# Performance work log

Hardware: AMD Instinct MI355X
Metric: run time of the kernel (lower is better)

## Reference

```python
import jax, jax.numpy as jnp
import numpy as np

EPS = 1e-4  # ridge term added to W W^T before inversion


def setup_inputs() -> dict:
    key = jax.random.key(0)
    k1, k2 = jax.random.split(key)
    B, F, C, D = 4096, 2048, 100, 16
    x = jax.random.normal(k1, (B, F), dtype=jnp.float32)
    # match torch reset_parameters: uniform(-stdv, stdv), stdv = 1/sqrt(F)
    stdv = 1.0 / np.sqrt(F)
    weight = jax.random.uniform(k2, (C, D, F), dtype=jnp.float32, minval=-stdv, maxval=stdv)
    return {"x": x, "weight": weight}


def reference(x, weight):
    # weight: [C, D, F], x: [B, F]
    C, D, F = weight.shape
    # per-capsule Gram matrix W W^T : [C, D, D]
    weight_caps = jnp.einsum('cdf,cef->cde', weight, weight)
    sigma = jnp.linalg.inv(weight_caps + EPS * jnp.eye(D, dtype=weight.dtype))
    # u[b,c,d] = <x_b, W_{c,d}>  (the x @ W^T projection of the original)
    u = jnp.einsum('bf,cdf->bcd', x, weight)
    # original chain: (u @ sigma @ W) @ x == u^T sigma u  (same math, no [B,C,F] temp)
    out = jnp.einsum('bcd,cde,bce->bc', u, sigma, u)
    return jnp.sqrt(out)
```

## Files before the change

### kernel.cpp

```cpp
#include <hip/hip_runtime.h>
#include <hip/hip_bf16.h>
#include <math.h>

#define F_DIM 2048
#define B_DIM 4096
#define C_DIM 100
#define D_DIM 16
#define N_DIM (C_DIM*D_DIM)
#define N_PAD 1664
#define RIDGE_EPS 1e-4f

typedef __attribute__((ext_vector_type(8))) short bf16x8;
typedef __attribute__((ext_vector_type(4))) float f32x4;

__device__ __forceinline__ void gload16(const void* g, void* l) {
  __builtin_amdgcn_global_load_lds(
      (const __attribute__((address_space(1))) void*)g,
      (__attribute__((address_space(3))) void*)l,
      16, 0, 0);
}

#define VM_BAR(N) asm volatile("s_waitcnt vmcnt(" #N ")\n\ts_barrier" ::: "memory")
#define LGKM_BAR() asm volatile("s_waitcnt lgkmcnt(0)\n\ts_barrier" ::: "memory")

__device__ __forceinline__ unsigned short f2bf(float f) {
  unsigned u = __float_as_uint(f);
  u += 0x7FFFu + ((u >> 16) & 1u);
  return (unsigned short)(u >> 16);
}

__global__ __launch_bounds__(256) void cvt_gram_kernel(
    const float* __restrict__ x, const float* __restrict__ w,
    unsigned short* __restrict__ xb, unsigned short* __restrict__ wb,
    float* __restrict__ sigma, int nx8, int nw8, int npad8) {
  __shared__ float part[4][64][4];
  __shared__ float G[16][17];
  __shared__ float IV[16][17];
  int t = threadIdx.x;
  if (blockIdx.x < C_DIM) {
    int c = blockIdx.x;
    int lane = t & 63, wid = t >> 6;
    const float* src = w + (size_t)c * (D_DIM * F_DIM)
                         + (size_t)(lane & 15) * F_DIM + ((lane >> 4) * 8) + wid * 512;
    f32x4 g = {0.f, 0.f, 0.f, 0.f};
#pragma unroll
    for (int kt = 0; kt < 16; ++kt) {
      float4 v0 = *(const float4*)(src + kt * 32);
      float4 v1 = *(const float4*)(src + kt * 32 + 4);
      bf16x8 f;
      f[0] = (short)f2bf(v0.x); f[1] = (short)f2bf(v0.y);
      f[2] = (short)f2bf(v0.z); f[3] = (short)f2bf(v0.w);
      f[4] = (short)f2bf(v1.x); f[5] = (short)f2bf(v1.y);
      f[6] = (short)f2bf(v1.z); f[7] = (short)f2bf(v1.w);
      g = __builtin_amdgcn_mfma_f32_16x16x32_bf16(f, f, g, 0, 0, 0);
    }
#pragma unroll
    for (int j = 0; j < 4; j++) part[wid][lane][j] = g[j];
    int d = t >> 4, e = t & 15;
    IV[d][e] = (d == e) ? 1.f : 0.f;
    __syncthreads();
    if (t < 64) {
      int col = t & 15;
#pragma unroll
      for (int j = 0; j < 4; j++) {
        int row = (t >> 4) * 4 + j;
        float s4 = part[0][t][j] + part[1][t][j] + part[2][t][j] + part[3][t][j];
        G[row][col] = s4 + (row == col ? RIDGE_EPS : 0.f);
      }
    }
    __syncthreads();
    for (int k = 0; k < 16; k++) {
      float piv = G[k][k];
      float gke = G[k][e];
      float ike = IV[k][e];
      float f   = G[d][k];
      float gde = G[d][e];
      float ide = IV[d][e];
      __syncthreads();
      if (d == k) {
        G[k][e]  = gke / piv;
        IV[k][e] = ike / piv;
      } else {
        G[d][e]  = gde - f * gke / piv;
        IV[d][e] = ide - f * ike / piv;
      }
      __syncthreads();
    }
    sigma[(size_t)c * 256 + t] = IV[d][e];
    return;
  }
  int i = (blockIdx.x - C_DIM) * 256 + t;
  const float* in; unsigned short* outp; int idx;
  if (i < nx8) { in = x; outp = xb; idx = i; }
  else {
    idx = i - nx8;
    if (idx >= nw8) {
      int idx3 = idx - nw8;
      if (idx3 < npad8) {
        uint4 z = {0, 0, 0, 0};
        *((uint4*)(wb + (size_t)N_DIM * F_DIM) + idx3) = z;
      }
      return;
    }
    in = w; outp = wb;
  }
  const float4* p = (const float4*)in + (size_t)idx * 2;
  float4 a = p[0], b = p[1];
  float v[8] = {a.x, a.y, a.z, a.w, b.x, b.y, b.z, b.w};
  union { unsigned short u16[8]; uint4 u4; } r;
#pragma unroll
  for (int j = 0; j < 8; j++) r.u16[j] = f2bf(v[j]);
  *((uint4*)outp + idx) = r.u4;
}

__global__ __launch_bounds__(512) void gemm_caps_kernel(
    const unsigned short* __restrict__ xb,
    const unsigned short* __restrict__ wb,
    const float* __restrict__ sigma,
    float* __restrict__ out)
{
  __shared__ __align__(16) unsigned char smem[67584];
  const int t = threadIdx.x;
  const int lane = t & 63;
  const int wid = t >> 6;
  const int wr = wid >> 2, wc = wid & 3;
  const int bid = blockIdx.x;
  const int swz = (bid & 7) * 52 + (bid >> 3);
  const int bn = swz % 13;
  const int bm = swz / 13;
  const int rowBase = bm * 128;
  const int colBase = bn * 128;

  unsigned char* buf0 = smem;
  unsigned char* buf1 = smem + 32768;

  const unsigned short* srcA[2]; unsigned qA[2];
  const unsigned short* srcB[2]; unsigned qB[2];
#pragma unroll
  for (int i = 0; i < 2; i++) {
    unsigned q = (unsigned)wid * 1024u + (unsigned)i * 8192u + (unsigned)lane * 16u;
    unsigned r = q >> 7, b = q & 127u;
    unsigned cb = b ^ ((r & 7u) << 4);
    qA[i] = q;
    srcA[i] = xb + (size_t)(rowBase + (int)r) * F_DIM + (cb >> 1);
    qB[i] = 16384u + q;
    srcB[i] = wb + (size_t)(colBase + (int)r) * F_DIM + (cb >> 1);
  }

  int aOff[4][2], bOff[2][2];
#pragma unroll
  for (int m = 0; m < 4; m++) {
    int r = wr * 64 + m * 16 + (lane & 15);
    int sw = (r & 7) << 4;
#pragma unroll
    for (int ks = 0; ks < 2; ks++) {
      int kb = ks * 64 + ((lane >> 4) << 4);
      aOff[m][ks] = r * 128 + (kb ^ sw);
    }
  }
#pragma unroll
  for (int n = 0; n < 2; n++) {
    int r = wc * 32 + n * 16 + (lane & 15);
    int sw = (r & 7) << 4;
#pragma unroll
    for (int ks = 0; ks < 2; ks++) {
      int kb = ks * 64 + ((lane >> 4) << 4);
      bOff[n][ks] = 16384 + r * 128 + (kb ^ sw);
    }
  }

  f32x4 acc[4][2];
#pragma unroll
  for (int m = 0; m < 4; m++)
#pragma unroll
    for (int n = 0; n < 2; n++)
      acc[m][n] = (f32x4){0.f, 0.f, 0.f, 0.f};

  auto stage = [&](unsigned char* buf, int kt) {
    const size_t koff = (size_t)kt * 64;
#pragma unroll
    for (int i = 0; i < 2; i++) gload16(srcA[i] + koff, buf + qA[i]);
#pragma unroll
    for (int i = 0; i < 2; i++) gload16(srcB[i] + koff, buf + qB[i]);
  };
  auto compute = [&](const unsigned char* buf) {
#pragma unroll
    for (int ks = 0; ks < 2; ks++) {
      bf16x8 a0 = *(const bf16x8*)(buf + aOff[0][ks]);
      bf16x8 a1 = *(const bf16x8*)(buf + aOff[1][ks]);
      bf16x8 a2 = *(const bf16x8*)(buf + aOff[2][ks]);
      bf16x8 a3 = *(const bf16x8*)(buf + aOff[3][ks]);
      bf16x8 b0 = *(const bf16x8*)(buf + bOff[0][ks]);
      bf16x8 b1 = *(const bf16x8*)(buf + bOff[1][ks]);
      acc[0][0] = __builtin_amdgcn_mfma_f32_16x16x32_bf16(a0, b0, acc[0][0], 0, 0, 0);
      acc[0][1] = __builtin_amdgcn_mfma_f32_16x16x32_bf16(a0, b1, acc[0][1], 0, 0, 0);
      acc[1][0] = __builtin_amdgcn_mfma_f32_16x16x32_bf16(a1, b0, acc[1][0], 0, 0, 0);
      acc[1][1] = __builtin_amdgcn_mfma_f32_16x16x32_bf16(a1, b1, acc[1][1], 0, 0, 0);
      acc[2][0] = __builtin_amdgcn_mfma_f32_16x16x32_bf16(a2, b0, acc[2][0], 0, 0, 0);
      acc[2][1] = __builtin_amdgcn_mfma_f32_16x16x32_bf16(a2, b1, acc[2][1], 0, 0, 0);
      acc[3][0] = __builtin_amdgcn_mfma_f32_16x16x32_bf16(a3, b0, acc[3][0], 0, 0, 0);
      acc[3][1] = __builtin_amdgcn_mfma_f32_16x16x32_bf16(a3, b1, acc[3][1], 0, 0, 0);
    }
  };

  stage(buf0, 0);
  for (int kt = 0; kt < 30; kt += 2) {
    stage(buf1, kt + 1);
    VM_BAR(4);
    compute(buf0);
    LGKM_BAR();
    stage(buf0, kt + 2);
    VM_BAR(4);
    compute(buf1);
    LGKM_BAR();
  }
  stage(buf1, 31);
  VM_BAR(4);
  compute(buf0);
  LGKM_BAR();
  VM_BAR(0);
  compute(buf1);
  LGKM_BAR();

  float* uT = (float*)smem;
#pragma unroll
  for (int m = 0; m < 4; m++)
#pragma unroll
    for (int n = 0; n < 2; n++)
#pragma unroll
      for (int j = 0; j < 4; j++) {
        int row = wr * 64 + m * 16 + ((lane >> 4) << 2) + j;
        int col = wc * 32 + n * 16 + (lane & 15);
        uT[row * 132 + col] = acc[m][n][j];
      }
  __syncthreads();
  const int capBase = bn * 8;
#pragma unroll
  for (int pp = 0; pp < 2; ++pp) {
    int pi = t + pp * 512;
    int row = pi & 127;
    int cl = __builtin_amdgcn_readfirstlane(pi >> 7);
    const float* uu = uT + row * 132 + cl * 16;
    f32x4 u0 = *(const f32x4*)(uu + 0);
    f32x4 u1 = *(const f32x4*)(uu + 4);
    f32x4 u2 = *(const f32x4*)(uu + 8);
    f32x4 u3 = *(const f32x4*)(uu + 12);
    float ur[16];
#pragma unroll
    for (int j = 0; j < 4; j++) { ur[j] = u0[j]; ur[4+j] = u1[j]; ur[8+j] = u2[j]; ur[12+j] = u3[j]; }
    int cap = capBase + cl;
    const float* s = sigma + (size_t)cap * 256;
    float qf = 0.f;
#pragma unroll
    for (int dd = 0; dd < 16; ++dd) {
      float td = 0.5f * s[dd * 16 + dd] * ur[dd];
#pragma unroll
      for (int ee = dd + 1; ee < 16; ++ee) td = fmaf(s[dd * 16 + ee], ur[ee], td);
      qf = fmaf(ur[dd], td, qf);
    }
    qf *= 2.f;
    if (cap < C_DIM)
      out[(size_t)(rowBase + row) * C_DIM + cap] = sqrtf(fmaxf(qf, 0.f));
  }
}

extern "C" void kernel_launch(void* const* d_in, const int* in_sizes, int n_in,
                              void* d_out, int out_size, void* d_ws, size_t ws_size,
                              hipStream_t stream) {
  const float* x = (const float*)d_in[0];
  const float* w = (const float*)d_in[1];
  float* out = (float*)d_out;

  unsigned short* xb = (unsigned short*)d_ws;
  unsigned short* wb = xb + (size_t)B_DIM * F_DIM;
  float* sigma = (float*)(wb + (size_t)N_PAD * F_DIM);

  int nx8 = B_DIM * F_DIM / 8;
  int nw8 = N_DIM * F_DIM / 8;
  int npad8 = (N_PAD - N_DIM) * F_DIM / 8;
  int nconv = nx8 + nw8 + npad8;
  int grid = C_DIM + (nconv + 255) / 256;
  cvt_gram_kernel<<<grid, 256, 0, stream>>>(x, w, xb, wb, sigma, nx8, nw8, npad8);
  gemm_caps_kernel<<<(B_DIM / 128) * (N_PAD / 128), 512, 0, stream>>>(xb, wb, sigma, out);
}
```

Baseline: 52.62 us.

## Split K across wave groups with 64x64 per-wave tiles and LDS reduction

Reassigns the 8 waves from a 2x4 grid of 64x32 output tiles into two K-halves, each covering the full 128x128 tile with a 2x2 grid of 64x64 per-wave tiles. Each wave now reads 4 A and 4 B fragments per K-step instead of 12 for the same MFMA count, which cuts LDS read traffic per MFMA. The two K-half partial sums are combined through a two-phase store-then-add into the shared uT buffer. In exchange each wave holds twice as many accumulator registers (64 floats), which may lower occupancy, and the epilogue gains an extra barrier and a read-modify-write pass over LDS.

```diff
diff --git a/kernel.cpp b/kernel.cpp
--- a/kernel.cpp
+++ b/kernel.cpp
@@ -123,7 +123,9 @@
   const int t = threadIdx.x;
   const int lane = t & 63;
   const int wid = t >> 6;
-  const int wr = wid >> 2, wc = wid & 3;
+  const int khalf = wid >> 2;
+  const int quad = wid & 3;
+  const int wr = quad >> 1, wc = quad & 1;
   const int bid = blockIdx.x;
   const int swz = (bid & 7) * 52 + (bid >> 3);
   const int bn = swz % 13;
@@ -147,33 +149,27 @@
     srcB[i] = wb + (size_t)(colBase + (int)r) * F_DIM + (cb >> 1);
   }
 
-  int aOff[4][2], bOff[2][2];
+  int aOff[4], bOff[4];
 #pragma unroll
   for (int m = 0; m < 4; m++) {
     int r = wr * 64 + m * 16 + (lane & 15);
     int sw = (r & 7) << 4;
-#pragma unroll
-    for (int ks = 0; ks < 2; ks++) {
-      int kb = ks * 64 + ((lane >> 4) << 4);
-      aOff[m][ks] = r * 128 + (kb ^ sw);
-    }
-  }
-#pragma unroll
-  for (int n = 0; n < 2; n++) {
-    int r = wc * 32 + n * 16 + (lane & 15);
+    int kb = khalf * 64 + ((lane >> 4) << 4);
+    aOff[m] = r * 128 + (kb ^ sw);
+  }
+#pragma unroll
+  for (int n = 0; n < 4; n++) {
+    int r = wc * 64 + n * 16 + (lane & 15);
     int sw = (r & 7) << 4;
-#pragma unroll
-    for (int ks = 0; ks < 2; ks++) {
-      int kb = ks * 64 + ((lane >> 4) << 4);
-      bOff[n][ks] = 16384 + r * 128 + (kb ^ sw);
-    }
-  }
-
-  f32x4 acc[4][2];
+    int kb = khalf * 64 + ((lane >> 4) << 4);
+    bOff[n] = 16384 + r * 128 + (kb ^ sw);
+  }
+
+  f32x4 acc[4][4];
 #pragma unroll
   for (int m = 0; m < 4; m++)
 #pragma unroll
-    for (int n = 0; n < 2; n++)
+    for (int n = 0; n < 4; n++)
       acc[m][n] = (f32x4){0.f, 0.f, 0.f, 0.f};
 
   auto stage = [&](unsigned char* buf, int kt) {
@@ -184,23 +180,30 @@
     for (int i = 0; i < 2; i++) gload16(srcB[i] + koff, buf + qB[i]);
   };
   auto compute = [&](const unsigned char* buf) {
-#pragma unroll
-    for (int ks = 0; ks < 2; ks++) {
-      bf16x8 a0 = *(const bf16x8*)(buf + aOff[0][ks]);
-      bf16x8 a1 = *(const bf16x8*)(buf + aOff[1][ks]);
-      bf16x8 a2 = *(const bf16x8*)(buf + aOff[2][ks]);
-      bf16x8 a3 = *(const bf16x8*)(buf + aOff[3][ks]);
-      bf16x8 b0 = *(const bf16x8*)(buf + bOff[0][ks]);
-      bf16x8 b1 = *(const bf16x8*)(buf + bOff[1][ks]);
-      acc[0][0] = __builtin_amdgcn_mfma_f32_16x16x32_bf16(a0, b0, acc[0][0], 0, 0, 0);
-      acc[0][1] = __builtin_amdgcn_mfma_f32_16x16x32_bf16(a0, b1, acc[0][1], 0, 0, 0);
-      acc[1][0] = __builtin_amdgcn_mfma_f32_16x16x32_bf16(a1, b0, acc[1][0], 0, 0, 0);
-      acc[1][1] = __builtin_amdgcn_mfma_f32_16x16x32_bf16(a1, b1, acc[1][1], 0, 0, 0);
-      acc[2][0] = __builtin_amdgcn_mfma_f32_16x16x32_bf16(a2, b0, acc[2][0], 0, 0, 0);
-      acc[2][1] = __builtin_amdgcn_mfma_f32_16x16x32_bf16(a2, b1, acc[2][1], 0, 0, 0);
-      acc[3][0] = __builtin_amdgcn_mfma_f32_16x16x32_bf16(a3, b0, acc[3][0], 0, 0, 0);
-      acc[3][1] = __builtin_amdgcn_mfma_f32_16x16x32_bf16(a3, b1, acc[3][1], 0, 0, 0);
-    }
+    bf16x8 a0 = *(const bf16x8*)(buf + aOff[0]);
+    bf16x8 a1 = *(const bf16x8*)(buf + aOff[1]);
+    bf16x8 a2 = *(const bf16x8*)(buf + aOff[2]);
+    bf16x8 a3 = *(const bf16x8*)(buf + aOff[3]);
+    bf16x8 b0 = *(const bf16x8*)(buf + bOff[0]);
+    bf16x8 b1 = *(const bf16x8*)(buf + bOff[1]);
+    bf16x8 b2 = *(const bf16x8*)(buf + bOff[2]);
+    bf16x8 b3 = *(const bf16x8*)(buf + bOff[3]);
+    acc[0][0] = __builtin_amdgcn_mfma_f32_16x16x32_bf16(a0, b0, acc[0][0], 0, 0, 0);
+    acc[0][1] = __builtin_amdgcn_mfma_f32_16x16x32_bf16(a0, b1, acc[0][1], 0, 0, 0);
+    acc[0][2] = __builtin_amdgcn_mfma_f32_16x16x32_bf16(a0, b2, acc[0][2], 0, 0, 0);
+    acc[0][3] = __builtin_amdgcn_mfma_f32_16x16x32_bf16(a0, b3, acc[0][3], 0, 0, 0);
+    acc[1][0] = __builtin_amdgcn_mfma_f32_16x16x32_bf16(a1, b0, acc[1][0], 0, 0, 0);
+    acc[1][1] = __builtin_amdgcn_mfma_f32_16x16x32_bf16(a1, b1, acc[1][1], 0, 0, 0);
+    acc[1][2] = __builtin_amdgcn_mfma_f32_16x16x32_bf16(a1, b2, acc[1][2], 0, 0, 0);
+    acc[1][3] = __builtin_amdgcn_mfma_f32_16x16x32_bf16(a1, b3, acc[1][3], 0, 0, 0);
+    acc[2][0] = __builtin_amdgcn_mfma_f32_16x16x32_bf16(a2, b0, acc[2][0], 0, 0, 0);
+    acc[2][1] = __builtin_amdgcn_mfma_f32_16x16x32_bf16(a2, b1, acc[2][1], 0, 0, 0);
+    acc[2][2] = __builtin_amdgcn_mfma_f32_16x16x32_bf16(a2, b2, acc[2][2], 0, 0, 0);
+    acc[2][3] = __builtin_amdgcn_mfma_f32_16x16x32_bf16(a2, b3, acc[2][3], 0, 0, 0);
+    acc[3][0] = __builtin_amdgcn_mfma_f32_16x16x32_bf16(a3, b0, acc[3][0], 0, 0, 0);
+    acc[3][1] = __builtin_amdgcn_mfma_f32_16x16x32_bf16(a3, b1, acc[3][1], 0, 0, 0);
+    acc[3][2] = __builtin_amdgcn_mfma_f32_16x16x32_bf16(a3, b2, acc[3][2], 0, 0, 0);
+    acc[3][3] = __builtin_amdgcn_mfma_f32_16x16x32_bf16(a3, b3, acc[3][3], 0, 0, 0);
   };
 
   stage(buf0, 0);
@@ -223,16 +226,31 @@
   LGKM_BAR();
 
   float* uT = (float*)smem;
-#pragma unroll
-  for (int m = 0; m < 4; m++)
-#pragma unroll
-    for (int n = 0; n < 2; n++)
-#pragma unroll
-      for (int j = 0; j < 4; j++) {
-        int row = wr * 64 + m * 16 + ((lane >> 4) << 2) + j;
-        int col = wc * 32 + n * 16 + (lane & 15);
-        uT[row * 132 + col] = acc[m][n][j];
-      }
+  if (khalf == 1) {
+#pragma unroll
+    for (int m = 0; m < 4; m++)
+#pragma unroll
+      for (int n = 0; n < 4; n++)
+#pragma unroll
+        for (int j = 0; j < 4; j++) {
+          int row = wr * 64 + m * 16 + ((lane >> 4) << 2) + j;
+          int col = wc * 64 + n * 16 + (lane & 15);
+          uT[row * 132 + col] = acc[m][n][j];
+        }
+  }
+  __syncthreads();
+  if (khalf == 0) {
+#pragma unroll
+    for (int m = 0; m < 4; m++)
+#pragma unroll
+      for (int n = 0; n < 4; n++)
+#pragma unroll
+        for (int j = 0; j < 4; j++) {
+          int row = wr * 64 + m * 16 + ((lane >> 4) << 2) + j;
+          int col = wc * 64 + n * 16 + (lane & 15);
+          uT[row * 132 + col] += acc[m][n][j];
+        }
+  }
   __syncthreads();
   const int capBase = bn * 8;
 #pragma unroll
```

Result: slower. 66.18 us (+25.8%).
